# Kernel tuning notes

Measured on AMD Instinct MI355X. Metric: run time of the kernel, lower is better.

## Reference

```python
import jax, jax.numpy as jnp
import numpy as np

EPS = 1e-6
BN_EPS = 1e-5
K = 20

def vn_linear(x, W):
    # x: (B, Cin, 3, ...), W: (Cout, Cin)
    return jnp.einsum('oc,bc...->bo...', W, x)

def vn_batchnorm(x, gamma, beta):
    # x: (B, C, 3, ...). BN (training-mode batch stats) over per-channel vector norms.
    n = jnp.linalg.norm(x, axis=2) + EPS               # (B, C, ...)
    red = (0,) + tuple(range(2, n.ndim))
    mu = n.mean(red, keepdims=True)
    var = ((n - mu) ** 2).mean(red, keepdims=True)     # biased var, as BatchNorm uses
    sh = (1, -1) + (1,) * (n.ndim - 2)
    nbn = (n - mu) / jnp.sqrt(var + BN_EPS) * gamma.reshape(sh) + beta.reshape(sh)
    return x / n[:, :, None] * nbn[:, :, None]

def vn_leaky(x, Wf, Wd, gamma, beta, ns):
    # VNLinearLeakyReLU: linear -> VN batchnorm -> direction-gated leaky relu
    p = vn_batchnorm(vn_linear(x, Wf), gamma, beta)
    d = vn_linear(x, Wd)
    dot = jnp.sum(p * d, axis=2, keepdims=True)
    dsq = jnp.sum(d * d, axis=2, keepdims=True) + EPS
    neg = p - (dot / dsq) * d
    return ns * p + (1.0 - ns) * jnp.where(dot >= 0, p, neg)

def graph_feature_cross(x, k):
    # x: (B, N, 3) -> edge features (B, 3, 3, N, k): [nbr - x, x, nbr x x]
    sq = jnp.sum(x * x, axis=-1)                        # (B, N)
    d2 = sq[:, :, None] + sq[:, None, :] - 2.0 * jnp.einsum('bnd,bmd->bnm', x, x)
    idx = jax.lax.top_k(-d2, k)[1]                      # (B, N, k) nearest incl. self
    nbr = jax.vmap(lambda pts, ind: pts[ind])(x, idx)   # (B, N, k, 3)
    c = jnp.broadcast_to(x[:, :, None, :], nbr.shape)
    cr = jnp.cross(nbr, c)
    feat = jnp.stack([nbr - c, c, cr], axis=3)          # (B, N, k, 3ch, 3)
    return jnp.transpose(feat, (0, 3, 4, 1, 2))         # (B, 3, 3, N, k)


def setup_inputs() -> dict:
    key = jax.random.key(0)
    ks = iter(jax.random.split(key, 40))
    def W(shape):
        return jax.random.normal(next(ks), shape, jnp.float32) * 0.05
    d = {'x': jax.random.normal(next(ks), (2, 2048, 3), jnp.float32)}
    d.update(
        Wf_pos=W((21, 3)), Wd_pos=W((21, 3)), g_pos=jnp.ones(21), be_pos=jnp.zeros(21),
        Wf1=W((21, 21)), Wd1=W((21, 21)), g1=jnp.ones(21), be1=jnp.zeros(21),
        Wf2=W((42, 21)), Wd2=W((42, 21)), g2=jnp.ones(42), be2=jnp.zeros(42),
        W3=W((170, 42)), g3=jnp.ones(170), be3=jnp.zeros(170),
        Ws1f=W((170, 340)), Ws1d=W((170, 340)), gs1=jnp.ones(170), bs1=jnp.zeros(170),
        Ws2f=W((85, 170)), Ws2d=W((85, 170)), gs2=jnp.ones(85), bs2=jnp.zeros(85),
        Wstd=W((3, 85)),
        Wt1=W((1020, 1020)), Wt2=W((1020, 1020)), Wt3=W((14450, 1020)), bt3=jnp.zeros(14450),
    )
    return d


def reference(x, Wf_pos, Wd_pos, g_pos, be_pos, Wf1, Wd1, g1, be1, Wf2, Wd2, g2, be2,
              W3, g3, be3, Ws1f, Ws1d, gs1, bs1, Ws2f, Ws2d, gs2, bs2, Wstd,
              Wt1, Wt2, Wt3, bt3):
    B, N, _ = x.shape
    feat = graph_feature_cross(x, K)                                   # (B,3,3,N,K)
    h = vn_leaky(feat, Wf_pos, Wd_pos, g_pos, be_pos, 0.0).mean(-1)    # (B,21,3,N) pool over k
    h = vn_leaky(h, Wf1, Wd1, g1, be1, 0.0)                            # (B,21,3,N)
    h = vn_leaky(h, Wf2, Wd2, g2, be2, 0.0)                            # (B,42,3,N)
    h = vn_batchnorm(vn_linear(h, W3), g3, be3)                        # (B,170,3,N)
    z = h.mean(-1)                                                     # (B,170,3)
    h = jnp.concatenate([h, jnp.broadcast_to(z[..., None], z.shape + (N,))], axis=1)  # (B,340,3,N)
    # VNStdFeature (normalize_frame=False, default negative_slope=0.2 inside)
    z0 = vn_leaky(h, Ws1f, Ws1d, gs1, bs1, 0.2)                        # (B,170,3,N)
    z0 = vn_leaky(z0, Ws2f, Ws2d, gs2, bs2, 0.2)                       # (B,85,3,N)
    z0 = vn_linear(z0, Wstd)                                           # (B,3,3,N)
    hs = jnp.einsum('bijn,bjkn->bikn', h, z0)                          # (B,340,3,N) invariant feats
    t = hs.reshape(B, 340 * 3, N)                                      # (B,1020,N)
    t = jax.nn.relu(jnp.einsum('oc,bcn->bon', Wt1, t))
    t = jax.nn.relu(jnp.einsum('oc,bcn->bon', Wt2, t))
    t = jnp.einsum('oc,bcn->bon', Wt3, t) + bt3[None, :, None]         # (B,14450,N)
    theta = t.reshape(B, 85, 170, N)
    return (z, theta)
```

## Files before the change

kernel.cpp:

```cpp
#include <hip/hip_runtime.h>
#include <cstdint>
#include <cstddef>

constexpr int   BB     = 2;
constexpr int   NN     = 2048;
constexpr int   KNB    = 20;
constexpr float EPS_   = 1e-6f;
constexpr float BNEPS_ = 1e-5f;
constexpr int   KPAD   = 1024;
constexpr int   NTK    = KPAD / 64;
constexpr int   MT3    = 57;
constexpr int   MPAD3  = MT3 * 256;

typedef __bf16 bf16x8 __attribute__((ext_vector_type(8)));
typedef float  f32x4  __attribute__((ext_vector_type(4)));
typedef unsigned short u16x8 __attribute__((ext_vector_type(8)));

typedef const void t_gvoid __attribute__((address_space(1)));
typedef void       t_lvoid __attribute__((address_space(3)));

__device__ __forceinline__ unsigned short f2bf(float f) {
  unsigned int u = __builtin_bit_cast(unsigned int, f);
  u += 0x7FFFu + ((u >> 16) & 1u);
  return (unsigned short)(u >> 16);
}

__global__ __launch_bounds__(256) void knn_kernel(const float* __restrict__ x,
                                                  int* __restrict__ idx) {
  __shared__ float4 pts[NN];
  const int b = blockIdx.x >> 9;
  const int tid = threadIdx.x;
  const float* xb = x + (size_t)b * NN * 3;
  for (int i = tid; i < NN; i += 256) {
    float px = xb[i * 3], py = xb[i * 3 + 1], pz = xb[i * 3 + 2];
    pts[i] = make_float4(px, py, pz, px * px + py * py + pz * pz);
  }
  __syncthreads();
  const int wave = tid >> 6, lane = tid & 63;
  const int q = (blockIdx.x & 511) * 4 + wave;
  const float4 qp = pts[q];

  float d[32];
  #pragma unroll
  for (int i = 0; i < 32; ++i) {
    const float4 p = pts[lane + 64 * i];
    d[i] = qp.w + p.w - 2.0f * (qp.x * p.x + qp.y * p.y + qp.z * p.z);
  }

  float m; int mi;
  auto rescan = [&]() {
    m = 3.4e38f; mi = 0;
    #pragma unroll
    for (int i = 0; i < 32; ++i)
      if (d[i] < m) { m = d[i]; mi = i; }
  };
  rescan();

  int* op = idx + ((size_t)b * NN + q) * KNB;
  for (int r = 0; r < KNB; ++r) {
    float bm = m; int bj = lane + 64 * mi;
    #pragma unroll
    for (int s = 32; s > 0; s >>= 1) {
      const float om = __shfl_xor(bm, s, 64);
      const int   oj = __shfl_xor(bj, s, 64);
      if (om < bm || (om == bm && oj < bj)) { bm = om; bj = oj; }
    }
    if (lane == 0) op[r] = bj;
    if ((bj & 63) == lane) {
      const int ii = bj >> 6;
      #pragma unroll
      for (int i = 0; i < 32; ++i)
        if (i == ii) d[i] = 3.4e38f;
      rescan();
    }
  }
}

__global__ void feat_kernel(const float* __restrict__ x, const int* __restrict__ idx,
                            float* __restrict__ feat) {
  const int i = blockIdx.x * 256 + threadIdx.x;
  if (i >= BB * NN * KNB) return;
  const int n = (i / KNB) % NN, b = i / (KNB * NN);
  const float* xb = x + (size_t)b * NN * 3;
  const int j = idx[i];
  const float cx = xb[n * 3], cy = xb[n * 3 + 1], cz = xb[n * 3 + 2];
  const float nx = xb[j * 3], ny = xb[j * 3 + 1], nz = xb[j * 3 + 2];
  float* f = feat + (size_t)i * 9;
  f[0] = nx - cx; f[1] = ny - cy; f[2] = nz - cz;
  f[3] = cx;      f[4] = cy;      f[5] = cz;
  f[6] = ny * cz - nz * cy;
  f[7] = nz * cx - nx * cz;
  f[8] = nx * cy - ny * cx;
}

__global__ void l1_stats_part(const float* __restrict__ feat, const float* __restrict__ Wf,
                              float* __restrict__ part) {
  const int o = blockIdx.x, g = blockIdx.y, tid = threadIdx.x;
  const float w0 = Wf[o * 3], w1 = Wf[o * 3 + 1], w2 = Wf[o * 3 + 2];
  const int M = BB * NN * KNB;
  const int chunk = M / 8;
  float s1 = 0.f, s2 = 0.f;
  for (int i = g * chunk + tid; i < (g + 1) * chunk; i += 256) {
    const float* f = feat + (size_t)i * 9;
    float p0 = w0 * f[0] + w1 * f[3] + w2 * f[6];
    float p1 = w0 * f[1] + w1 * f[4] + w2 * f[7];
    float p2 = w0 * f[2] + w1 * f[5] + w2 * f[8];
    float nr = sqrtf(p0 * p0 + p1 * p1 + p2 * p2) + EPS_;
    s1 += nr; s2 += nr * nr;
  }
  __shared__ float rA[256], rB[256];
  rA[tid] = s1; rB[tid] = s2; __syncthreads();
  for (int off = 128; off > 0; off >>= 1) {
    if (tid < off) { rA[tid] += rA[tid + off]; rB[tid] += rB[tid + off]; }
    __syncthreads();
  }
  if (tid == 0) {
    part[(o * 8 + g) * 2]     = rA[0];
    part[(o * 8 + g) * 2 + 1] = rB[0];
  }
}

__global__ void l1_stats_fin(const float* __restrict__ part, const float* __restrict__ gamma,
                             float* __restrict__ stats) {
  const int o = threadIdx.x;
  if (o >= 21) return;
  const int M = BB * NN * KNB;
  float s1 = 0.f, s2 = 0.f;
  for (int g = 0; g < 8; ++g) { s1 += part[(o * 8 + g) * 2]; s2 += part[(o * 8 + g) * 2 + 1]; }
  float mu = s1 / M;
  float var = fmaxf(s2 / M - mu * mu, 0.f);
  stats[2 * o] = mu;
  stats[2 * o + 1] = gamma[o] / sqrtf(var + BNEPS_);
}

__global__ void l1_final_kernel(const float* __restrict__ feat, const float* __restrict__ Wf,
                                const float* __restrict__ Wd, const float* __restrict__ stats,
                                const float* __restrict__ beta, float* __restrict__ h1) {
  const int o = blockIdx.y, b = blockIdx.z;
  const int n = blockIdx.x * 256 + threadIdx.x;
  const float wf0 = Wf[o * 3], wf1 = Wf[o * 3 + 1], wf2 = Wf[o * 3 + 2];
  const float wd0 = Wd[o * 3], wd1 = Wd[o * 3 + 1], wd2 = Wd[o * 3 + 2];
  const float mu = stats[2 * o], sc = stats[2 * o + 1], be = beta[o];
  const float* fb = feat + ((size_t)(b * NN + n)) * KNB * 9;
  float a0 = 0.f, a1 = 0.f, a2 = 0.f;
  for (int k = 0; k < KNB; ++k) {
    const float* f = fb + k * 9;
    float p0 = wf0 * f[0] + wf1 * f[3] + wf2 * f[6];
    float p1 = wf0 * f[1] + wf1 * f[4] + wf2 * f[7];
    float p2 = wf0 * f[2] + wf1 * f[5] + wf2 * f[8];
    float d0 = wd0 * f[0] + wd1 * f[3] + wd2 * f[6];
    float d1 = wd0 * f[1] + wd1 * f[4] + wd2 * f[7];
    float d2 = wd0 * f[2] + wd1 * f[5] + wd2 * f[8];
    float nr = sqrtf(p0 * p0 + p1 * p1 + p2 * p2) + EPS_;
    float fac = ((nr - mu) * sc + be) / nr;
    p0 *= fac; p1 *= fac; p2 *= fac;
    float dot = p0 * d0 + p1 * d1 + p2 * d2;
    if (dot < 0.f) {
      float g = dot / (d0 * d0 + d1 * d1 + d2 * d2 + EPS_);
      p0 -= g * d0; p1 -= g * d1; p2 -= g * d2;
    }
    a0 += p0; a1 += p1; a2 += p2;
  }
  const size_t base = ((size_t)(b * 21 + o) * 3) * NN + n;
  h1[base]          = a0 * (1.f / KNB);
  h1[base + NN]     = a1 * (1.f / KNB);
  h1[base + 2 * NN] = a2 * (1.f / KNB);
}

__global__ void zbias_kernel(const float* __restrict__ zbuf, const float* __restrict__ Wf,
                             const float* __restrict__ Wd, float* __restrict__ zbf,
                             float* __restrict__ zbd, int Cout, int CinFull, int Cz) {
  const int bj = blockIdx.x;
  const int b = bj / 3, j = bj % 3;
  const int o = threadIdx.x;
  if (o >= Cout) return;
  const int off = CinFull - Cz;
  float sf = 0.f, sd = 0.f;
  for (int cz = 0; cz < Cz; ++cz) {
    const float zv = zbuf[((size_t)b * 170 + cz) * 3 + j];
    sf += Wf[(size_t)o * CinFull + off + cz] * zv;
    sd += Wd[(size_t)o * CinFull + off + cz] * zv;
  }
  zbf[(size_t)bj * Cout + o] = sf;
  zbd[(size_t)bj * Cout + o] = sd;
}

template <int HAS_D, int CONCAT_Z>
__global__ __launch_bounds__(256) void vn_lin_fast(
    const float* __restrict__ in, const float* __restrict__ Wf, const float* __restrict__ Wd,
    const float* __restrict__ zbf, const float* __restrict__ zbd,
    float* __restrict__ pout, float* __restrict__ dout,
    int Cin, int CinFull, int Cout) {
  __shared__ float wsh[(HAS_D ? 2 : 1) * 16 * 340];
  float* wfs = wsh;
  float* wds = HAS_D ? (wsh + 16 * 340) : wsh;
  const int tid = threadIdx.x;
  const int nt = blockIdx.x, ot = blockIdx.y;
  const int b = blockIdx.z / 3, j = blockIdx.z % 3;

  for (int i = tid; i < 16 * Cin; i += 256) {
    const int ol = i / Cin, c = i - ol * Cin;
    const int o = ot * 16 + ol;
    wfs[ol * Cin + c] = (o < Cout) ? Wf[(size_t)o * CinFull + c] : 0.f;
    if (HAS_D) wds[ol * Cin + c] = (o < Cout) ? Wd[(size_t)o * CinFull + c] : 0.f;
  }
  __syncthreads();

  const int lane = tid & 63, og = tid >> 6;
  const int n0 = nt * 256 + lane * 4;
  const float* ibase = in + ((size_t)b * Cin * 3 + j) * NN + n0;

  f32x4 accf[4], accd[4];
  #pragma unroll
  for (int oo = 0; oo < 4; ++oo) {
    float bf = 0.f, bd = 0.f;
    if (CONCAT_Z) {
      const int o = ot * 16 + og * 4 + oo;
      if (o < Cout) {
        bf = zbf[(size_t)blockIdx.z * Cout + o];
        bd = zbd[(size_t)blockIdx.z * Cout + o];
      }
    }
    accf[oo] = (f32x4){bf, bf, bf, bf};
    accd[oo] = (f32x4){bd, bd, bd, bd};
  }

  #pragma unroll 4
  for (int c = 0; c < Cin; ++c) {
    const f32x4 v = *reinterpret_cast<const f32x4*>(ibase + (size_t)c * 3 * NN);
    #pragma unroll
    for (int oo = 0; oo < 4; ++oo) {
      const float wf = wfs[(og * 4 + oo) * Cin + c];
      accf[oo] += wf * v;
      if (HAS_D) {
        const float wd = wds[(og * 4 + oo) * Cin + c];
        accd[oo] += wd * v;
      }
    }
  }

  #pragma unroll
  for (int oo = 0; oo < 4; ++oo) {
    const int o = ot * 16 + og * 4 + oo;
    if (o < Cout) {
      const size_t ob = ((size_t)(b * Cout + o) * 3 + j) * NN + n0;
      *reinterpret_cast<f32x4*>(pout + ob) = accf[oo];
      if (HAS_D) *reinterpret_cast<f32x4*>(dout + ob) = accd[oo];
    }
  }
}

__global__ void bn_stats_kernel(const float* __restrict__ p, const float* __restrict__ gamma,
                                float* __restrict__ stats, int Cout) {
  const int o = blockIdx.x, tid = threadIdx.x;
  const int M = BB * NN;
  float s1 = 0.f, s2 = 0.f;
  for (int i = tid; i < M; i += 256) {
    const int b = i >> 11, n = i & (NN - 1);
    const size_t base = (((size_t)(b * Cout + o)) * 3) * NN + n;
    float p0 = p[base], p1 = p[base + NN], p2 = p[base + 2 * NN];
    float nr = sqrtf(p0 * p0 + p1 * p1 + p2 * p2) + EPS_;
    s1 += nr; s2 += nr * nr;
  }
  __shared__ float rA[256], rB[256];
  rA[tid] = s1; rB[tid] = s2; __syncthreads();
  for (int off = 128; off > 0; off >>= 1) {
    if (tid < off) { rA[tid] += rA[tid + off]; rB[tid] += rB[tid + off]; }
    __syncthreads();
  }
  if (tid == 0) {
    float mu = rA[0] / M;
    float var = fmaxf(rB[0] / M - mu * mu, 0.f);
    stats[2 * o] = mu;
    stats[2 * o + 1] = gamma[o] / sqrtf(var + BNEPS_);
  }
}

template <int GATE>
__global__ void vn_gate_kernel(const float* __restrict__ p, const float* __restrict__ d,
                               const float* __restrict__ stats, const float* __restrict__ beta,
                               float* __restrict__ out, int Cout, float ns) {
  const int o = blockIdx.y, b = blockIdx.z;
  const int n = blockIdx.x * 256 + threadIdx.x;
  const size_t base = (((size_t)(b * Cout + o)) * 3) * NN + n;
  float p0 = p[base], p1 = p[base + NN], p2 = p[base + 2 * NN];
  const float nr = sqrtf(p0 * p0 + p1 * p1 + p2 * p2) + EPS_;
  const float fac = ((nr - stats[2 * o]) * stats[2 * o + 1] + beta[o]) / nr;
  p0 *= fac; p1 *= fac; p2 *= fac;
  float o0 = p0, o1 = p1, o2 = p2;
  if (GATE) {
    const float d0 = d[base], d1 = d[base + NN], d2 = d[base + 2 * NN];
    const float dot = p0 * d0 + p1 * d1 + p2 * d2;
    if (dot < 0.f) {
      const float g = dot / (d0 * d0 + d1 * d1 + d2 * d2 + EPS_);
      o0 = p0 - g * d0; o1 = p1 - g * d1; o2 = p2 - g * d2;
    }
    o0 = ns * p0 + (1.f - ns) * o0;
    o1 = ns * p1 + (1.f - ns) * o1;
    o2 = ns * p2 + (1.f - ns) * o2;
  }
  out[base] = o0; out[base + NN] = o1; out[base + 2 * NN] = o2;
}

__global__ void zmean_kernel(const float* __restrict__ h4, float* __restrict__ zbuf,
                             float* __restrict__ outz) {
  const int oj = blockIdx.x;
  const int b = blockIdx.y;
  const int tid = threadIdx.x;
  const float* src = h4 + ((size_t)b * 510 + oj) * NN;
  float s = 0.f;
  for (int n = tid; n < NN; n += 256) s += src[n];
  __shared__ float r[256];
  r[tid] = s; __syncthreads();
  for (int off = 128; off > 0; off >>= 1) {
    if (tid < off) r[tid] += r[tid + off];
    __syncthreads();
  }
  if (tid == 0) {
    float m = r[0] / NN;
    zbuf[(size_t)b * 510 + oj] = m;
    outz[(size_t)b * 510 + oj] = m;
  }
}

__global__ void hs_kernel(const float* __restrict__ h4, const float* __restrict__ zbuf,
                          const float* __restrict__ z0f, unsigned short* __restrict__ t0) {
  const int n = blockIdx.x;
  const int b = blockIdx.z;
  const int tid = threadIdx.x;
  __shared__ float zf[9];
  __shared__ float hcol[512];
  __shared__ float zcol[512];
  if (tid < 9) zf[tid] = z0f[(((size_t)(b * 3 + tid / 3)) * 3 + (tid % 3)) * NN + n];
  for (int i = tid; i < 510; i += 256) {
    hcol[i] = h4[((size_t)b * 510 + i) * NN + n];
    zcol[i] = zbuf[(size_t)b * 510 + i];
  }
  __syncthreads();
  unsigned short* trow = t0 + ((size_t)b * NN + n) * KPAD;
  for (int c = tid; c < KPAD; c += 256) {
    if (c >= 1020) { trow[c] = 0; continue; }
    const int i = c / 3, kv = c % 3;
    float acc = 0.f;
    #pragma unroll
    for (int j = 0; j < 3; ++j) {
      const float hv = (i < 170) ? hcol[i * 3 + j] : zcol[(i - 170) * 3 + j];
      acc += hv * zf[j * 3 + kv];
    }
    trow[c] = f2bf(acc);
  }
}

__global__ void wconv_kernel(const float* __restrict__ W, unsigned short* __restrict__ out,
                             int M, int Kv, size_t total8) {
  size_t i = (size_t)blockIdx.x * 256 + threadIdx.x;
  const size_t stride = (size_t)gridDim.x * 256;
  for (; i < total8; i += stride) {
    const size_t e = i * 8;
    const int k = (int)(e & (KPAD - 1));
    const int o = (int)(e >> 10);
    u16x8 v;
    if (o < M && k + 8 <= Kv) {
      const float* src = W + (size_t)o * Kv + k;
      #pragma unroll
      for (int t = 0; t < 8; ++t) v[t] = f2bf(src[t]);
    } else {
      #pragma unroll
      for (int t = 0; t < 8; ++t) {
        const int kk = k + t;
        v[t] = (o < M && kk < Kv) ? f2bf(W[(size_t)o * Kv + kk]) : (unsigned short)0;
      }
    }
    *reinterpret_cast<u16x8*>(out + e) = v;
  }
}

template <int RELU>
__global__ __launch_bounds__(256) void gemm_kernel(
    const unsigned short* __restrict__ A, const unsigned short* __restrict__ Bmat,
    unsigned short* __restrict__ outB, int M) {
  __shared__ __align__(16) unsigned short lA[2][128 * 64];
  __shared__ __align__(16) unsigned short lB[2][128 * 64];
  const int tid = threadIdx.x;
  const int nwg = gridDim.x, q = nwg >> 3;
  const int orig = blockIdx.x;
  const int swz = (orig & 7) * q + (orig >> 3);
  const int ntile = swz & 15;
  const int mtile = (swz >> 4) & 7;
  const int b = swz >> 7;
  const int lane = tid & 63, w = tid >> 6;
  const int wm = w >> 1, wn = w & 1;
  const int lrow = lane & 15, lgrp = lane >> 4;

  const unsigned short* Abase = A + (size_t)mtile * 128 * KPAD;
  const unsigned short* Bbase = Bmat + ((size_t)b * NN + (size_t)ntile * 128) * KPAD;

  const int rowS = tid >> 3;
  const int scol = ((tid & 7) * 8) ^ ((rowS & 7) * 8);
  const int wb8  = __builtin_amdgcn_readfirstlane(tid & 192) * 8;

  f32x4 acc[4][4];
  #pragma unroll
  for (int mi = 0; mi < 4; ++mi)
    #pragma unroll
    for (int ni = 0; ni < 4; ++ni) acc[mi][ni] = (f32x4){0.f, 0.f, 0.f, 0.f};

  auto stage = [&](int bufi, int kt) {
    const int kof = kt * 64;
    #pragma unroll
    for (int r = 0; r < 4; ++r) {
      __builtin_amdgcn_global_load_lds(
          (t_gvoid*)(Abase + (size_t)(r * 32 + rowS) * KPAD + kof + scol),
          (t_lvoid*)&lA[bufi][r * 2048 + wb8], 16, 0, 0);
      __builtin_amdgcn_global_load_lds(
          (t_gvoid*)(Bbase + (size_t)(r * 32 + rowS) * KPAD + kof + scol),
          (t_lvoid*)&lB[bufi][r * 2048 + wb8], 16, 0, 0);
    }
  };

  stage(0, 0);
  for (int kt = 0; kt < NTK; ++kt) {
    const int cur = kt & 1;
    if (kt + 1 < NTK) {
      stage(cur ^ 1, kt + 1);
      asm volatile("s_waitcnt vmcnt(8)" ::: "memory");
    } else {
      asm volatile("s_waitcnt vmcnt(0)" ::: "memory");
    }
    asm volatile("s_barrier" ::: "memory");

    bf16x8 af[4][2], bfr[4][2];
    #pragma unroll
    for (int mi = 0; mi < 4; ++mi) {
      const int ra = wm * 64 + mi * 16 + lrow;
      const int rb = wn * 64 + mi * 16 + lrow;
      #pragma unroll
      for (int kk = 0; kk < 2; ++kk) {
        af[mi][kk]  = *reinterpret_cast<const bf16x8*>(
            &lA[cur][ra * 64 + ((kk * 32 + lgrp * 8) ^ ((ra & 7) * 8))]);
        bfr[mi][kk] = *reinterpret_cast<const bf16x8*>(
            &lB[cur][rb * 64 + ((kk * 32 + lgrp * 8) ^ ((rb & 7) * 8))]);
      }
    }
    #pragma unroll
    for (int kk = 0; kk < 2; ++kk)
      #pragma unroll
      for (int mi = 0; mi < 4; ++mi)
        #pragma unroll
        for (int ni = 0; ni < 4; ++ni)
          acc[mi][ni] = __builtin_amdgcn_mfma_f32_16x16x32_bf16(af[mi][kk], bfr[ni][kk],
                                                                acc[mi][ni], 0, 0, 0);
    asm volatile("s_barrier" ::: "memory");
  }

  const int fr_col = lane & 15;
  const int fr_rowb = (lane >> 4) * 4;
  #pragma unroll
  for (int mi = 0; mi < 4; ++mi) {
    const int rowb = mtile * 128 + wm * 64 + mi * 16 + fr_rowb;
    #pragma unroll
    for (int ni = 0; ni < 4; ++ni) {
      const int col = ntile * 128 + wn * 64 + ni * 16 + fr_col;
      ushort4 v;
      if (rowb < M) {
        float u0 = acc[mi][ni][0], u1 = acc[mi][ni][1], u2 = acc[mi][ni][2], u3 = acc[mi][ni][3];
        if (RELU) { u0 = fmaxf(u0, 0.f); u1 = fmaxf(u1, 0.f); u2 = fmaxf(u2, 0.f); u3 = fmaxf(u3, 0.f); }
        v.x = f2bf(u0); v.y = f2bf(u1); v.z = f2bf(u2); v.w = f2bf(u3);
      } else {
        v.x = v.y = v.z = v.w = 0;
      }
      *reinterpret_cast<ushort4*>(outB + ((size_t)b * NN + col) * KPAD + rowb) = v;
    }
  }
}

__global__ __launch_bounds__(512, 2) void gemm256_kernel(
    const unsigned short* __restrict__ A, const unsigned short* __restrict__ Bmat,
    float* __restrict__ outF, const float* __restrict__ bias, int M, int MT) {
  __shared__ __align__(16) unsigned short lA[2][256 * 64];
  __shared__ __align__(16) unsigned short lB[2][256 * 64];
  const int tid = threadIdx.x;
  const int nwg = gridDim.x, q = nwg >> 3;
  const int orig = blockIdx.x;
  const int swz = (orig & 7) * q + (orig >> 3);
  const int ntile = swz & 7;
  const int rem = swz >> 3;
  const int mtile = rem % MT;
  const int b = rem / MT;
  const int lane = tid & 63, w = tid >> 6;
  const int wm = w >> 2, wn = w & 3;
  const int lrow = lane & 15, lgrp = lane >> 4;

  const unsigned short* Abase = A + (size_t)mtile * 256 * KPAD;
  const unsigned short* Bbase = Bmat + ((size_t)b * NN + (size_t)ntile * 256) * KPAD;

  const int rowS = tid >> 3;
  const int scol = ((tid & 7) * 8) ^ ((rowS & 7) * 8);
  const int wb8  = __builtin_amdgcn_readfirstlane((tid & 448) >> 6) * 512;

  f32x4 acc[8][4];
  #pragma unroll
  for (int mi = 0; mi < 8; ++mi)
    #pragma unroll
    for (int ni = 0; ni < 4; ++ni) acc[mi][ni] = (f32x4){0.f, 0.f, 0.f, 0.f};

  auto stage = [&](int bufi, int kt) {
    const int kof = kt * 64;
    #pragma unroll
    for (int r = 0; r < 4; ++r) {
      __builtin_amdgcn_global_load_lds(
          (t_gvoid*)(Abase + (size_t)(r * 64 + rowS) * KPAD + kof + scol),
          (t_lvoid*)&lA[bufi][r * 4096 + wb8], 16, 0, 0);
      __builtin_amdgcn_global_load_lds(
          (t_gvoid*)(Bbase + (size_t)(r * 64 + rowS) * KPAD + kof + scol),
          (t_lvoid*)&lB[bufi][r * 4096 + wb8], 16, 0, 0);
    }
  };

  stage(0, 0);
  for (int kt = 0; kt < NTK; ++kt) {
    const int cur = kt & 1;
    if (kt + 1 < NTK) {
      stage(cur ^ 1, kt + 1);
      asm volatile("s_waitcnt vmcnt(8)" ::: "memory");
    } else {
      asm volatile("s_waitcnt vmcnt(0)" ::: "memory");
    }
    asm volatile("s_barrier" ::: "memory");

    #pragma unroll
    for (int kk = 0; kk < 2; ++kk) {
      bf16x8 af[8], bfr[4];
      #pragma unroll
      for (int mi = 0; mi < 8; ++mi) {
        const int ra = wm * 128 + mi * 16 + lrow;
        af[mi] = *reinterpret_cast<const bf16x8*>(
            &lA[cur][ra * 64 + ((kk * 32 + lgrp * 8) ^ ((ra & 7) * 8))]);
      }
      #pragma unroll
      for (int ni = 0; ni < 4; ++ni) {
        const int rb = wn * 64 + ni * 16 + lrow;
        bfr[ni] = *reinterpret_cast<const bf16x8*>(
            &lB[cur][rb * 64 + ((kk * 32 + lgrp * 8) ^ ((rb & 7) * 8))]);
      }
      #pragma unroll
      for (int mi = 0; mi < 8; ++mi)
        #pragma unroll
        for (int ni = 0; ni < 4; ++ni)
          acc[mi][ni] = __builtin_amdgcn_mfma_f32_16x16x32_bf16(af[mi], bfr[ni],
                                                                acc[mi][ni], 0, 0, 0);
    }
    asm volatile("s_barrier" ::: "memory");
  }

  const int fr_col = lane & 15;
  const int fr_rowb = (lane >> 4) * 4;
  #pragma unroll
  for (int mi = 0; mi < 8; ++mi) {
    const int rowb = mtile * 256 + wm * 128 + mi * 16 + fr_rowb;
    #pragma unroll
    for (int ni = 0; ni < 4; ++ni) {
      const int col = ntile * 256 + wn * 64 + ni * 16 + fr_col;
      #pragma unroll
      for (int r = 0; r < 4; ++r) {
        const int rr = rowb + r;
        if (rr < M) outF[((size_t)b * M + rr) * NN + col] = acc[mi][ni][r] + bias[rr];
      }
    }
  }
}

extern "C" void kernel_launch(void* const* d_in, const int* in_sizes, int n_in,
                              void* d_out, int out_size, void* d_ws, size_t ws_size,
                              hipStream_t stream) {
  const float* x      = (const float*)d_in[0];
  const float* Wf_pos = (const float*)d_in[1];
  const float* Wd_pos = (const float*)d_in[2];
  const float* g_pos  = (const float*)d_in[3];
  const float* be_pos = (const float*)d_in[4];
  const float* Wf1    = (const float*)d_in[5];
  const float* Wd1    = (const float*)d_in[6];
  const float* g1     = (const float*)d_in[7];
  const float* be1    = (const float*)d_in[8];
  const float* Wf2    = (const float*)d_in[9];
  const float* Wd2    = (const float*)d_in[10];
  const float* g2     = (const float*)d_in[11];
  const float* be2    = (const float*)d_in[12];
  const float* W3     = (const float*)d_in[13];
  const float* g3     = (const float*)d_in[14];
  const float* be3    = (const float*)d_in[15];
  const float* Ws1f   = (const float*)d_in[16];
  const float* Ws1d   = (const float*)d_in[17];
  const float* gs1    = (const float*)d_in[18];
  const float* bs1    = (const float*)d_in[19];
  const float* Ws2f   = (const float*)d_in[20];
  const float* Ws2d   = (const float*)d_in[21];
  const float* gs2    = (const float*)d_in[22];
  const float* bs2    = (const float*)d_in[23];
  const float* Wstd   = (const float*)d_in[24];
  const float* Wt1    = (const float*)d_in[25];
  const float* Wt2    = (const float*)d_in[26];
  const float* Wt3    = (const float*)d_in[27];
  const float* bt3    = (const float*)d_in[28];
  (void)in_sizes; (void)n_in; (void)out_size; (void)ws_size;

  float* out = (float*)d_out;
  float* out_theta = out + 1020;

  char* ws = (char*)d_ws;
  size_t off = 0;
  auto alloc = [&](size_t bytes) -> void* {
    void* p = (void*)(ws + off);
    off += (bytes + 255) & ~(size_t)255;
    return p;
  };
  int*            idx  = (int*)           alloc((size_t)BB * NN * KNB * 4);
  float*          feat = (float*)         alloc((size_t)BB * NN * KNB * 9 * 4);
  float*          stats= (float*)         alloc(1024 * 4);
  float*          part = (float*)         alloc(2048 * 4);
  float*          h1   = (float*)         alloc((size_t)BB * 21 * 3 * NN * 4);
  float*          h2   = (float*)         alloc((size_t)BB * 21 * 3 * NN * 4);
  float*          h3   = (float*)         alloc((size_t)BB * 42 * 3 * NN * 4);
  float*          h4   = (float*)         alloc((size_t)BB * 170 * 3 * NN * 4);
  float*          zbuf = (float*)         alloc((size_t)BB * 170 * 3 * 4);
  float*          pbuf = (float*)         alloc((size_t)BB * 170 * 3 * NN * 4);
  float*          dbuf = (float*)         alloc((size_t)BB * 170 * 3 * NN * 4);
  float*          z0a  = (float*)         alloc((size_t)BB * 170 * 3 * NN * 4);
  float*          z0b  = (float*)         alloc((size_t)BB * 85 * 3 * NN * 4);
  float*          z0f  = (float*)         alloc((size_t)BB * 3 * 3 * NN * 4);
  float*          zbf  = (float*)         alloc((size_t)6 * 170 * 4);
  float*          zbd  = (float*)         alloc((size_t)6 * 170 * 4);
  unsigned short* W1b  = (unsigned short*)alloc((size_t)1024 * KPAD * 2);
  unsigned short* W2b  = (unsigned short*)alloc((size_t)1024 * KPAD * 2);
  unsigned short* W3b  = (unsigned short*)alloc((size_t)MPAD3 * KPAD * 2);
  unsigned short* t0   = (unsigned short*)alloc((size_t)BB * NN * KPAD * 2);
  unsigned short* t1   = (unsigned short*)alloc((size_t)BB * NN * KPAD * 2);
  unsigned short* t2   = t0;

  knn_kernel<<<BB * 512, 256, 0, stream>>>(x, idx);
  feat_kernel<<<(BB * NN * KNB + 255) / 256, 256, 0, stream>>>(x, idx, feat);
  l1_stats_part<<<dim3(21, 8), 256, 0, stream>>>(feat, Wf_pos, part);
  l1_stats_fin<<<1, 64, 0, stream>>>(part, g_pos, stats);
  l1_final_kernel<<<dim3(8, 21, BB), 256, 0, stream>>>(feat, Wf_pos, Wd_pos, stats, be_pos, h1);

  vn_lin_fast<1, 0><<<dim3(8, 2, BB * 3), 256, 0, stream>>>(h1, Wf1, Wd1, nullptr, nullptr, pbuf, dbuf, 21, 21, 21);
  bn_stats_kernel<<<21, 256, 0, stream>>>(pbuf, g1, stats, 21);
  vn_gate_kernel<1><<<dim3(8, 21, BB), 256, 0, stream>>>(pbuf, dbuf, stats, be1, h2, 21, 0.0f);

  vn_lin_fast<1, 0><<<dim3(8, 3, BB * 3), 256, 0, stream>>>(h2, Wf2, Wd2, nullptr, nullptr, pbuf, dbuf, 21, 21, 42);
  bn_stats_kernel<<<42, 256, 0, stream>>>(pbuf, g2, stats, 42);
  vn_gate_kernel<1><<<dim3(8, 42, BB), 256, 0, stream>>>(pbuf, dbuf, stats, be2, h3, 42, 0.0f);

  vn_lin_fast<0, 0><<<dim3(8, 11, BB * 3), 256, 0, stream>>>(h3, W3, nullptr, nullptr, nullptr, pbuf, nullptr, 42, 42, 170);
  bn_stats_kernel<<<170, 256, 0, stream>>>(pbuf, g3, stats, 170);
  vn_gate_kernel<0><<<dim3(8, 170, BB), 256, 0, stream>>>(pbuf, nullptr, stats, be3, h4, 170, 0.0f);

  zmean_kernel<<<dim3(510, BB), 256, 0, stream>>>(h4, zbuf, out);

  zbias_kernel<<<6, 256, 0, stream>>>(zbuf, Ws1f, Ws1d, zbf, zbd, 170, 340, 170);
  vn_lin_fast<1, 1><<<dim3(8, 11, BB * 3), 256, 0, stream>>>(h4, Ws1f, Ws1d, zbf, zbd, pbuf, dbuf, 170, 340, 170);
  bn_stats_kernel<<<170, 256, 0, stream>>>(pbuf, gs1, stats, 170);
  vn_gate_kernel<1><<<dim3(8, 170, BB), 256, 0, stream>>>(pbuf, dbuf, stats, bs1, z0a, 170, 0.2f);

  vn_lin_fast<1, 0><<<dim3(8, 6, BB * 3), 256, 0, stream>>>(z0a, Ws2f, Ws2d, nullptr, nullptr, pbuf, dbuf, 170, 170, 85);
  bn_stats_kernel<<<85, 256, 0, stream>>>(pbuf, gs2, stats, 85);
  vn_gate_kernel<1><<<dim3(8, 85, BB), 256, 0, stream>>>(pbuf, dbuf, stats, bs2, z0b, 85, 0.2f);

  vn_lin_fast<0, 0><<<dim3(8, 1, BB * 3), 256, 0, stream>>>(z0b, Wstd, nullptr, nullptr, nullptr, z0f, nullptr, 85, 85, 3);

  hs_kernel<<<dim3(NN, 1, BB), 256, 0, stream>>>(h4, zbuf, z0f, t0);

  wconv_kernel<<<512, 256, 0, stream>>>(Wt1, W1b, 1020, 1020, (size_t)1024 * KPAD / 8);
  wconv_kernel<<<512, 256, 0, stream>>>(Wt2, W2b, 1020, 1020, (size_t)1024 * KPAD / 8);
  wconv_kernel<<<2048, 256, 0, stream>>>(Wt3, W3b, 14450, 1020, (size_t)MPAD3 * KPAD / 8);

  gemm_kernel<1><<<256, 256, 0, stream>>>(W1b, t0, t1, 1020);
  gemm_kernel<1><<<256, 256, 0, stream>>>(W2b, t1, t2, 1020);
  gemm256_kernel<<<8 * MT3 * BB, 512, 0, stream>>>(W3b, t2, out_theta, bt3, 14450, MT3);
}
```

Measured before the change: 563.7 us.

## Fuse BN norm statistics into VN linear and z-mean into gate kernel

The VN linear kernel now computes all three vector components per thread so it can form per-point norms and emit per-block partial sums of norm and norm², which removes the separate bn_stats pass over the output. The gate kernel reduces those 32 partials itself, and for layer 3 it also emits per-block partial sums for the z mean, which replaces the full zmean pass over h4. The work per thread along the point axis drops from 4 to 2 points, changing the grid shape. This removes several kernel launches and full re-reads of the intermediates, but every gate thread now redundantly sums 64 partial values.

```diff
diff --git a/kernel.cpp b/kernel.cpp
--- a/kernel.cpp
+++ b/kernel.cpp
@@ -14,6 +14,7 @@
 
 typedef __bf16 bf16x8 __attribute__((ext_vector_type(8)));
 typedef float  f32x4  __attribute__((ext_vector_type(4)));
+typedef float  f32x2  __attribute__((ext_vector_type(2)));
 typedef unsigned short u16x8 __attribute__((ext_vector_type(8)));
 
 typedef const void t_gvoid __attribute__((address_space(1)));
@@ -185,18 +186,17 @@
   zbd[(size_t)bj * Cout + o] = sd;
 }
 
-template <int HAS_D, int CONCAT_Z>
-__global__ __launch_bounds__(256) void vn_lin_fast(
+template <int HAS_D, int CONCAT_Z, int WRITE_STATS>
+__global__ __launch_bounds__(256) void vn_lin_fused(
     const float* __restrict__ in, const float* __restrict__ Wf, const float* __restrict__ Wd,
     const float* __restrict__ zbf, const float* __restrict__ zbd,
-    float* __restrict__ pout, float* __restrict__ dout,
+    float* __restrict__ pout, float* __restrict__ dout, float* __restrict__ bpart,
     int Cin, int CinFull, int Cout) {
   __shared__ float wsh[(HAS_D ? 2 : 1) * 16 * 340];
   float* wfs = wsh;
   float* wds = HAS_D ? (wsh + 16 * 340) : wsh;
   const int tid = threadIdx.x;
-  const int nt = blockIdx.x, ot = blockIdx.y;
-  const int b = blockIdx.z / 3, j = blockIdx.z % 3;
+  const int nt = blockIdx.x, ot = blockIdx.y, b = blockIdx.z;
 
   for (int i = tid; i < 16 * Cin; i += 256) {
     const int ol = i / Cin, c = i - ol * Cin;
@@ -207,34 +207,41 @@
   __syncthreads();
 
   const int lane = tid & 63, og = tid >> 6;
-  const int n0 = nt * 256 + lane * 4;
-  const float* ibase = in + ((size_t)b * Cin * 3 + j) * NN + n0;
-
-  f32x4 accf[4], accd[4];
+  const int n0 = nt * 128 + lane * 2;
+  const float* ibase = in + ((size_t)b * Cin * 3) * NN + n0;
+
+  f32x2 pf[4][3], pd[4][3];
   #pragma unroll
-  for (int oo = 0; oo < 4; ++oo) {
-    float bf = 0.f, bd = 0.f;
-    if (CONCAT_Z) {
-      const int o = ot * 16 + og * 4 + oo;
-      if (o < Cout) {
-        bf = zbf[(size_t)blockIdx.z * Cout + o];
-        bd = zbd[(size_t)blockIdx.z * Cout + o];
-      }
-    }
-    accf[oo] = (f32x4){bf, bf, bf, bf};
-    accd[oo] = (f32x4){bd, bd, bd, bd};
-  }
-
-  #pragma unroll 4
+  for (int oo = 0; oo < 4; ++oo)
+    #pragma unroll
+    for (int j = 0; j < 3; ++j) {
+      float bf = 0.f, bd = 0.f;
+      if (CONCAT_Z) {
+        const int o = ot * 16 + og * 4 + oo;
+        if (o < Cout) {
+          bf = zbf[(size_t)(b * 3 + j) * Cout + o];
+          bd = zbd[(size_t)(b * 3 + j) * Cout + o];
+        }
+      }
+      pf[oo][j] = (f32x2){bf, bf};
+      pd[oo][j] = (f32x2){bd, bd};
+    }
+
+  #pragma unroll 2
   for (int c = 0; c < Cin; ++c) {
-    const f32x4 v = *reinterpret_cast<const f32x4*>(ibase + (size_t)c * 3 * NN);
+    f32x2 v[3];
+    #pragma unroll
+    for (int j = 0; j < 3; ++j)
+      v[j] = *reinterpret_cast<const f32x2*>(ibase + ((size_t)c * 3 + j) * NN);
     #pragma unroll
     for (int oo = 0; oo < 4; ++oo) {
       const float wf = wfs[(og * 4 + oo) * Cin + c];
-      accf[oo] += wf * v;
+      #pragma unroll
+      for (int j = 0; j < 3; ++j) pf[oo][j] += wf * v[j];
       if (HAS_D) {
         const float wd = wds[(og * 4 + oo) * Cin + c];
-        accd[oo] += wd * v;
+        #pragma unroll
+        for (int j = 0; j < 3; ++j) pd[oo][j] += wd * v[j];
       }
     }
   }
@@ -243,49 +250,62 @@
   for (int oo = 0; oo < 4; ++oo) {
     const int o = ot * 16 + og * 4 + oo;
     if (o < Cout) {
-      const size_t ob = ((size_t)(b * Cout + o) * 3 + j) * NN + n0;
-      *reinterpret_cast<f32x4*>(pout + ob) = accf[oo];
-      if (HAS_D) *reinterpret_cast<f32x4*>(dout + ob) = accd[oo];
-    }
-  }
-}
-
-__global__ void bn_stats_kernel(const float* __restrict__ p, const float* __restrict__ gamma,
-                                float* __restrict__ stats, int Cout) {
-  const int o = blockIdx.x, tid = threadIdx.x;
+      const size_t ob = ((size_t)(b * Cout + o) * 3) * NN + n0;
+      #pragma unroll
+      for (int j = 0; j < 3; ++j) {
+        *reinterpret_cast<f32x2*>(pout + ob + (size_t)j * NN) = pf[oo][j];
+        if (HAS_D) *reinterpret_cast<f32x2*>(dout + ob + (size_t)j * NN) = pd[oo][j];
+      }
+    }
+  }
+
+  if (WRITE_STATS) {
+    #pragma unroll
+    for (int oo = 0; oo < 4; ++oo) {
+      float s1 = 0.f, s2 = 0.f;
+      #pragma unroll
+      for (int t = 0; t < 2; ++t) {
+        const float nr = sqrtf(pf[oo][0][t] * pf[oo][0][t] + pf[oo][1][t] * pf[oo][1][t] +
+                               pf[oo][2][t] * pf[oo][2][t]) + EPS_;
+        s1 += nr; s2 += nr * nr;
+      }
+      #pragma unroll
+      for (int s = 32; s > 0; s >>= 1) {
+        s1 += __shfl_xor(s1, s, 64);
+        s2 += __shfl_xor(s2, s, 64);
+      }
+      const int o = ot * 16 + og * 4 + oo;
+      if (lane == 0 && o < Cout) {
+        bpart[(o * 32 + b * 16 + nt) * 2]     = s1;
+        bpart[(o * 32 + b * 16 + nt) * 2 + 1] = s2;
+      }
+    }
+  }
+}
+
+template <int GATE, int ZPART>
+__global__ void vn_gate2(const float* __restrict__ p, const float* __restrict__ d,
+                         const float* __restrict__ bpart, const float* __restrict__ gamma,
+                         const float* __restrict__ beta, float* __restrict__ out,
+                         float* __restrict__ zpart, int Cout, float ns) {
+  const int o = blockIdx.y, b = blockIdx.z;
+  const int n = blockIdx.x * 256 + threadIdx.x;
   const int M = BB * NN;
   float s1 = 0.f, s2 = 0.f;
-  for (int i = tid; i < M; i += 256) {
-    const int b = i >> 11, n = i & (NN - 1);
-    const size_t base = (((size_t)(b * Cout + o)) * 3) * NN + n;
-    float p0 = p[base], p1 = p[base + NN], p2 = p[base + 2 * NN];
-    float nr = sqrtf(p0 * p0 + p1 * p1 + p2 * p2) + EPS_;
-    s1 += nr; s2 += nr * nr;
-  }
-  __shared__ float rA[256], rB[256];
-  rA[tid] = s1; rB[tid] = s2; __syncthreads();
-  for (int off = 128; off > 0; off >>= 1) {
-    if (tid < off) { rA[tid] += rA[tid + off]; rB[tid] += rB[tid + off]; }
-    __syncthreads();
-  }
-  if (tid == 0) {
-    float mu = rA[0] / M;
-    float var = fmaxf(rB[0] / M - mu * mu, 0.f);
-    stats[2 * o] = mu;
-    stats[2 * o + 1] = gamma[o] / sqrtf(var + BNEPS_);
-  }
-}
-
-template <int GATE>
-__global__ void vn_gate_kernel(const float* __restrict__ p, const float* __restrict__ d,
-                               const float* __restrict__ stats, const float* __restrict__ beta,
-                               float* __restrict__ out, int Cout, float ns) {
-  const int o = blockIdx.y, b = blockIdx.z;
-  const int n = blockIdx.x * 256 + threadIdx.x;
+  #pragma unroll 8
+  for (int i = 0; i < 32; ++i) {
+    s1 += bpart[(o * 32 + i) * 2];
+    s2 += bpart[(o * 32 + i) * 2 + 1];
+  }
+  const float mu = s1 / M;
+  const float var = fmaxf(s2 / M - mu * mu, 0.f);
+  const float sc = gamma[o] / sqrtf(var + BNEPS_);
+  const float be = beta[o];
+
   const size_t base = (((size_t)(b * Cout + o)) * 3) * NN + n;
   float p0 = p[base], p1 = p[base + NN], p2 = p[base + 2 * NN];
   const float nr = sqrtf(p0 * p0 + p1 * p1 + p2 * p2) + EPS_;
-  const float fac = ((nr - stats[2 * o]) * stats[2 * o + 1] + beta[o]) / nr;
+  const float fac = ((nr - mu) * sc + be) / nr;
   p0 *= fac; p1 *= fac; p2 *= fac;
   float o0 = p0, o1 = p1, o2 = p2;
   if (GATE) {
@@ -300,27 +320,36 @@
     o2 = ns * p2 + (1.f - ns) * o2;
   }
   out[base] = o0; out[base + NN] = o1; out[base + 2 * NN] = o2;
-}
-
-__global__ void zmean_kernel(const float* __restrict__ h4, float* __restrict__ zbuf,
-                             float* __restrict__ outz) {
-  const int oj = blockIdx.x;
-  const int b = blockIdx.y;
-  const int tid = threadIdx.x;
-  const float* src = h4 + ((size_t)b * 510 + oj) * NN;
+
+  if (ZPART) {
+    float t0 = o0, t1 = o1, t2 = o2;
+    #pragma unroll
+    for (int s = 32; s > 0; s >>= 1) {
+      t0 += __shfl_xor(t0, s, 64);
+      t1 += __shfl_xor(t1, s, 64);
+      t2 += __shfl_xor(t2, s, 64);
+    }
+    __shared__ float zsh[3][4];
+    const int lane = threadIdx.x & 63, wv = threadIdx.x >> 6;
+    if (lane == 0) { zsh[0][wv] = t0; zsh[1][wv] = t1; zsh[2][wv] = t2; }
+    __syncthreads();
+    if (threadIdx.x < 3) {
+      const float s = zsh[threadIdx.x][0] + zsh[threadIdx.x][1] + zsh[threadIdx.x][2] + zsh[threadIdx.x][3];
+      zpart[(size_t)(((b * Cout + o) * 3 + threadIdx.x)) * 8 + blockIdx.x] = s;
+    }
+  }
+}
+
+__global__ void zmean_fin(const float* __restrict__ zpart, float* __restrict__ zbuf,
+                          float* __restrict__ outz) {
+  const int idx = blockIdx.x * 256 + threadIdx.x;
+  if (idx >= BB * 510) return;
   float s = 0.f;
-  for (int n = tid; n < NN; n += 256) s += src[n];
-  __shared__ float r[256];
-  r[tid] = s; __syncthreads();
-  for (int off = 128; off > 0; off >>= 1) {
-    if (tid < off) r[tid] += r[tid + off];
-    __syncthreads();
-  }
-  if (tid == 0) {
-    float m = r[0] / NN;
-    zbuf[(size_t)b * 510 + oj] = m;
-    outz[(size_t)b * 510 + oj] = m;
-  }
+  #pragma unroll
+  for (int i = 0; i < 8; ++i) s += zpart[(size_t)idx * 8 + i];
+  const float m = s / NN;
+  zbuf[idx] = m;
+  outz[idx] = m;
 }
 
 __global__ void hs_kernel(const float* __restrict__ h4, const float* __restrict__ zbuf,
@@ -618,6 +647,8 @@
   float*          feat = (float*)         alloc((size_t)BB * NN * KNB * 9 * 4);
   float*          stats= (float*)         alloc(1024 * 4);
   float*          part = (float*)         alloc(2048 * 4);
+  float*          bpart= (float*)         alloc((size_t)170 * 32 * 2 * 4);
+  float*          zpart= (float*)         alloc((size_t)510 * BB * 8 * 4);
   float*          h1   = (float*)         alloc((size_t)BB * 21 * 3 * NN * 4);
   float*          h2   = (float*)         alloc((size_t)BB * 21 * 3 * NN * 4);
   float*          h3   = (float*)         alloc((size_t)BB * 42 * 3 * NN * 4);
@@ -643,30 +674,25 @@
   l1_stats_fin<<<1, 64, 0, stream>>>(part, g_pos, stats);
   l1_final_kernel<<<dim3(8, 21, BB), 256, 0, stream>>>(feat, Wf_pos, Wd_pos, stats, be_pos, h1);
 
-  vn_lin_fast<1, 0><<<dim3(8, 2, BB * 3), 256, 0, stream>>>(h1, Wf1, Wd1, nullptr, nullptr, pbuf, dbuf, 21, 21, 21);
-  bn_stats_kernel<<<21, 256, 0, stream>>>(pbuf, g1, stats, 21);
-  vn_gate_kernel<1><<<dim3(8, 21, BB), 256, 0, stream>>>(pbuf, dbuf, stats, be1, h2, 21, 0.0f);
-
-  vn_lin_fast<1, 0><<<dim3(8, 3, BB * 3), 256, 0, stream>>>(h2, Wf2, Wd2, nullptr, nullptr, pbuf, dbuf, 21, 21, 42);
-  bn_stats_kernel<<<42, 256, 0, stream>>>(pbuf, g2, stats, 42);
-  vn_gate_kernel<1><<<dim3(8, 42, BB), 256, 0, stream>>>(pbuf, dbuf, stats, be2, h3, 42, 0.0f);
-
-  vn_lin_fast<0, 0><<<dim3(8, 11, BB * 3), 256, 0, stream>>>(h3, W3, nullptr, nullptr, nullptr, pbuf, nullptr, 42, 42, 170);
-  bn_stats_kernel<<<170, 256, 0, stream>>>(pbuf, g3, stats, 170);
-  vn_gate_kernel<0><<<dim3(8, 170, BB), 256, 0, stream>>>(pbuf, nullptr, stats, be3, h4, 170, 0.0f);
-
-  zmean_kernel<<<dim3(510, BB), 256, 0, stream>>>(h4, zbuf, out);
+  vn_lin_fused<1, 0, 1><<<dim3(16, 2, BB), 256, 0, stream>>>(h1, Wf1, Wd1, nullptr, nullptr, pbuf, dbuf, bpart, 21, 21, 21);
+  vn_gate2<1, 0><<<dim3(8, 21, BB), 256, 0, stream>>>(pbuf, dbuf, bpart, g1, be1, h2, nullptr, 21, 0.0f);
+
+  vn_lin_fused<1, 0, 1><<<dim3(16, 3, BB), 256, 0, stream>>>(h2, Wf2, Wd2, nullptr, nullptr, pbuf, dbuf, bpart, 21, 21, 42);
+  vn_gate2<1, 0><<<dim3(8, 42, BB), 256, 0, stream>>>(pbuf, dbuf, bpart, g2, be2, h3, nullptr, 42, 0.0f);
+
+  vn_lin_fused<0, 0, 1><<<dim3(16, 11, BB), 256, 0, stream>>>(h3, W3, nullptr, nullptr, nullptr, pbuf, nullptr, bpart, 42, 42, 170);
+  vn_gate2<0, 1><<<dim3(8, 170, BB), 256, 0, stream>>>(pbuf, nullptr, bpart, g3, be3, h4, zpart, 170, 0.0f);
+
+  zmean_fin<<<(BB * 510 + 255) / 256, 256, 0, stream>>>(zpart, zbuf, out);
 
   zbias_kernel<<<6, 256, 0, stream>>>(zbuf, Ws1f, Ws1d, zbf, zbd, 170, 340, 170);
-  vn_lin_fast<1, 1><<<dim3(8, 11, BB * 3), 256, 0, stream>>>(h4, Ws1f, Ws1d, zbf, zbd, pbuf, dbuf, 170, 340, 170);
-  bn_stats_kernel<<<170, 256, 0, stream>>>(pbuf, gs1, stats, 170);
-  vn_gate_kernel<1><<<dim3(8, 170, BB), 256, 0, stream>>>(pbuf, dbuf, stats, bs1, z0a, 170, 0.2f);
-
-  vn_lin_fast<1, 0><<<dim3(8, 6, BB * 3), 256, 0, stream>>>(z0a, Ws2f, Ws2d, nullptr, nullptr, pbuf, dbuf, 170, 170, 85);
-  bn_stats_kernel<<<85, 256, 0, stream>>>(pbuf, gs2, stats, 85);
-  vn_gate_kernel<1><<<dim3(8, 85, BB), 256, 0, stream>>>(pbuf, dbuf, stats, bs2, z0b, 85, 0.2f);
-
-  vn_lin_fast<0, 0><<<dim3(8, 1, BB * 3), 256, 0, stream>>>(z0b, Wstd, nullptr, nullptr, nullptr, z0f, nullptr, 85, 85, 3);
+  vn_lin_fused<1, 1, 1><<<dim3(16, 11, BB), 256, 0, stream>>>(h4, Ws1f, Ws1d, zbf, zbd, pbuf, dbuf, bpart, 170, 340, 170);
+  vn_gate2<1, 0><<<dim3(8, 170, BB), 256, 0, stream>>>(pbuf, dbuf, bpart, gs1, bs1, z0a, nullptr, 170, 0.2f);
+
+  vn_lin_fused<1, 0, 1><<<dim3(16, 6, BB), 256, 0, stream>>>(z0a, Ws2f, Ws2d, nullptr, nullptr, pbuf, dbuf, bpart, 170, 170, 85);
+  vn_gate2<1, 0><<<dim3(8, 85, BB), 256, 0, stream>>>(pbuf, dbuf, bpart, gs2, bs2, z0b, nullptr, 85, 0.2f);
+
+  vn_lin_fused<0, 0, 0><<<dim3(16, 1, BB), 256, 0, stream>>>(z0b, Wstd, nullptr, nullptr, nullptr, z0f, nullptr, nullptr, 85, 85, 3);
 
   hs_kernel<<<dim3(NN, 1, BB), 256, 0, stream>>>(h4, zbuf, z0f, t0);
 
```

Measured after the change: 586.2 us. 1.04x slower.
